# Kernel tuning notes

Hardware: AMD Instinct MI355X
Metric: run time of the kernel (lower is better)

The kernel has to match this reference:

```python
import jax, jax.numpy as jnp
import numpy as np

N = 100000   # nodes
E = 1200000  # edges
FIN = 128    # in_channels
H = 64       # hidden_channels
OUT = 1      # out_channels


def setup_inputs() -> dict:
    key = jax.random.key(0)
    ks = jax.random.split(key, 12)
    s = 0.05
    return {
        "x": jax.random.normal(ks[0], (N, FIN), jnp.float32),
        "edge_index": jax.random.randint(ks[1], (2, E), 0, N, dtype=jnp.int64),
        "W0": jax.random.normal(ks[2], (FIN, H), jnp.float32) * s,
        "b0": jnp.zeros((H,), jnp.float32),
        "W1": jax.random.normal(ks[3], (H, H), jnp.float32) * s,
        "b1": jnp.zeros((H,), jnp.float32),
        "W2": jax.random.normal(ks[4], (H, OUT), jnp.float32) * s,
        "b2": jnp.zeros((OUT,), jnp.float32),
        "Wm1": jax.random.normal(ks[5], (OUT, H), jnp.float32) * s,
        "bm1": jnp.zeros((H,), jnp.float32),
        "Wm2": jax.random.normal(ks[6], (H, OUT), jnp.float32) * s,
        "bm2": jnp.zeros((OUT,), jnp.float32),
    }


def reference(x, edge_index, W0, b0, W1, b1, W2, b2, Wm1, bm1, Wm2, bm2):
    # GCNConv (PyG default): add self-loops, symmetric normalization D^-1/2 A D^-1/2
    loop = jnp.arange(N, dtype=edge_index.dtype)
    src = jnp.concatenate([edge_index[0], loop])  # [E+N]
    dst = jnp.concatenate([edge_index[1], loop])
    deg = jax.ops.segment_sum(jnp.ones(E + N, jnp.float32), dst, num_segments=N)
    dinv = jax.lax.rsqrt(deg)  # deg >= 1 thanks to self-loops
    norm = dinv[src] * dinv[dst]  # [E+N]

    def conv(h, W, b):
        h = h @ W  # [N, d_out]
        msg = h[src] * norm[:, None]  # gather + scale, [E+N, d_out]
        return jax.ops.segment_sum(msg, dst, num_segments=N) + b

    h = jax.nn.relu(conv(x, W0, b0))   # input layer (dropout is identity in eval)
    h = jax.nn.relu(conv(h, W1, b1))   # hidden layer
    h = conv(h, W2, b2)                # output GCN layer -> [N, OUT]
    # MLP head
    h = jax.nn.relu(h @ Wm1 + bm1) @ Wm2 + bm2
    return h
```

## Files before the change

kernel.cpp:

```cpp
#include <hip/hip_runtime.h>
#include <hip/hip_fp16.h>
#include <math.h>

#define ELL_CAP 48
#define NBUCK 391
#define BCAP 3584

typedef _Float16 half8 __attribute__((ext_vector_type(8)));
typedef float floatx4 __attribute__((ext_vector_type(4)));


__device__ __forceinline__ __half2 u2h(unsigned u) {
  __half2 h; __builtin_memcpy(&h, &u, 4); return h;
}
__device__ __forceinline__ unsigned h2u(__half2 h) {
  unsigned u; __builtin_memcpy(&u, &h, 4); return u;
}


__global__ __launch_bounds__(1024) void k_bucket(const int* __restrict__ src,
                                                 const int* __restrict__ dst,
                                                 int* __restrict__ cursors,
                                                 int* __restrict__ buckets, int E) {
  __shared__ int hist[NBUCK];
  __shared__ int base[NBUCK];
  const int tid = threadIdx.x;
  for (int i = tid; i < NBUCK; i += 1024) hist[i] = 0;
  __syncthreads();

  const long s0 = (long)blockIdx.x * E / gridDim.x;
  const long s1 = (long)(blockIdx.x + 1) * E / gridDim.x;

  for (long e = s0 + tid; e < s1; e += 1024) atomicAdd(&hist[dst[e] >> 8], 1);
  __syncthreads();

  for (int i = tid; i < NBUCK; i += 1024) {
    int c = hist[i];
    base[i] = (c > 0) ? atomicAdd(&cursors[i], c) : 0;
    hist[i] = 0;
  }
  __syncthreads();

  for (long e = s0 + tid; e < s1; e += 1024) {
    int s = src[e], d = dst[e];
    int b = d >> 8;
    int pos = base[b] + atomicAdd(&hist[b], 1);
    if (pos < BCAP) buckets[(long)b * BCAP + pos] = ((d & 255) << 24) | s;
  }
}


__global__ __launch_bounds__(256) void k_ellbuild(const int* __restrict__ buckets,
                                                  const int* __restrict__ cursors,
                                                  int* __restrict__ cnt,
                                                  int* __restrict__ ell,
                                                  float* __restrict__ dinv,
                                                  int* __restrict__ remap,
                                                  __half* __restrict__ zrow, int n) {
  __shared__ int cnt_l[256];
  __shared__ int ell_l[256 * ELL_CAP];
  __shared__ int dh[64];
  __shared__ int dbase[64];
  const int b = blockIdx.x, tid = threadIdx.x;
  cnt_l[tid] = 0;
  if (tid < 64) dh[tid] = 0;
  if (b == 0 && tid < 64) zrow[tid] = __float2half(0.f);
  __syncthreads();

  int m = cursors[b];
  if (m > BCAP) m = BCAP;
  const int* bk = buckets + (long)b * BCAP;
  for (int i = tid; i < m; i += 256) {
    int p = bk[i];
    int ld = ((unsigned)p) >> 24;
    int pos = atomicAdd(&cnt_l[ld], 1);
    if (pos < ELL_CAP) ell_l[ld * ELL_CAP + pos] = p & 0xFFFFFF;
  }
  __syncthreads();

  const int d0 = b << 8;
  const int node = d0 + tid;
  const int rows = min(256, n - d0);
  int c = 0;
  if (tid < rows) {
    c = cnt_l[tid];
    if (c > ELL_CAP) c = ELL_CAP;
    cnt[node] = c;
    dinv[node] = 1.0f / sqrtf((float)(c + 1));
    atomicAdd(&dh[c], 1);
  }
  __syncthreads();
  if (tid == 0) {
    int s = 0;
    for (int i = 0; i < 64; ++i) { dbase[i] = s; s += dh[i]; }
  }
  __syncthreads();
  if (tid < rows) {
    int r = atomicAdd(&dbase[c], 1);
    remap[d0 + r] = node;
  }

  const int lim4 = rows * ELL_CAP / 4;
  int4* dst4 = (int4*)(ell + (long)d0 * ELL_CAP);
  const int4* src4 = (const int4*)ell_l;
  for (int i = tid; i < lim4; i += 256) dst4[i] = src4[i];
}


template <int K, bool RELU, bool IN_HALF>
__global__ __launch_bounds__(256) void k_gemm_mfma(const void* __restrict__ Xv,
                                                   const float* __restrict__ W,
                                                   const float* __restrict__ dinv,
                                                   __half* __restrict__ out, int n) {
  constexpr int SP = K + 8;
  constexpr int NS = K / 32;
  __shared__ __half Wl[64 * SP];
  const int tx = threadIdx.x;

  for (int idx = tx; idx < (K / 2) * 64; idx += 256) {
    int k2 = idx >> 6, col = idx & 63;
    __half2 h = __floats2half2_rn(W[(2 * k2) * 64 + col], W[(2 * k2 + 1) * 64 + col]);
    *(__half2*)&Wl[col * SP + 2 * k2] = h;
  }
  __syncthreads();

  const int lane = tx & 63;
  const int l15 = lane & 15;
  const int quad = lane >> 4;
  const long base = (long)blockIdx.x * 64 + (tx >> 6) * 16;

  long arow = base + l15;
  if (arow >= n) arow = n - 1;
  const float* Xf = (const float*)Xv;
  const __half* Xh = (const __half*)Xv;

  half8 afrag[NS];
#pragma unroll
  for (int s = 0; s < NS; ++s) {
    if constexpr (IN_HALF) {
      afrag[s] = *(const half8*)&Xh[arow * K + s * 32 + quad * 8];
    } else {
      float4 lo = *(const float4*)&Xf[arow * K + s * 32 + quad * 8];
      float4 hi = *(const float4*)&Xf[arow * K + s * 32 + quad * 8 + 4];
      half8 a;
      a[0] = (_Float16)lo.x; a[1] = (_Float16)lo.y;
      a[2] = (_Float16)lo.z; a[3] = (_Float16)lo.w;
      a[4] = (_Float16)hi.x; a[5] = (_Float16)hi.y;
      a[6] = (_Float16)hi.z; a[7] = (_Float16)hi.w;
      afrag[s] = a;
    }
    if (RELU) {
      unsigned short* u = (unsigned short*)&afrag[s];
#pragma unroll
      for (int j = 0; j < 8; ++j) u[j] = (u[j] & 0x8000) ? (unsigned short)0 : u[j];
    }
  }

  floatx4 acc[4];
#pragma unroll
  for (int t = 0; t < 4; ++t) acc[t] = (floatx4){0.f, 0.f, 0.f, 0.f};

#pragma unroll
  for (int s = 0; s < NS; ++s) {
#pragma unroll
    for (int t = 0; t < 4; ++t) {
      half8 bfrag = *(const half8*)&Wl[(t * 16 + l15) * SP + s * 32 + quad * 8];
      acc[t] = __builtin_amdgcn_mfma_f32_16x16x32_f16(afrag[s], bfrag, acc[t], 0, 0, 0);
    }
  }

#pragma unroll
  for (int r = 0; r < 4; ++r) {
    long node = base + quad * 4 + r;
    if (node < n) {
      float dv = dinv[node];
#pragma unroll
      for (int t = 0; t < 4; ++t)
        out[node * 64 + t * 16 + l15] = __float2half(acc[t][r] * dv);
    }
  }
}


template <typename EPI>
__device__ __forceinline__ void gather8(const __half* __restrict__ hs,
                                        const int* __restrict__ ell,
                                        const int* __restrict__ cnt,
                                        const float* __restrict__ dinv,
                                        const int* __restrict__ remap,
                                        int n, EPI epi) {
  const int tid = threadIdx.x;
  const int lane = tid & 63;
  const int l8 = lane & 7;
  const int wave = (blockIdx.x * 256 + tid) >> 6;
  const int slot = wave * 8 + (lane >> 3);
  const bool alive = slot < n;
  const int nd = alive ? remap[slot] : 0;
  const int c = alive ? cnt[nd] : 0;
  const float di = alive ? dinv[nd] : 0.f;
  const int* row = &ell[(long)nd * ELL_CAP];

  int s0 = (l8 < c) ? row[l8] : n;
  int s1 = (8 + l8 < c) ? row[8 + l8] : n;

  int cm = c;
  cm = max(cm, __shfl_xor(cm, 8, 64));
  cm = max(cm, __shfl_xor(cm, 16, 64));
  cm = max(cm, __shfl_xor(cm, 32, 64));
  const int nph = (cm + 7) >> 3;

  float accf[8];
  {
    float4 v = alive ? *(const float4*)&hs[(long)nd * 64 + l8 * 8]
                     : make_float4(0.f, 0.f, 0.f, 0.f);
    const unsigned* up = (const unsigned*)&v;
#pragma unroll
    for (int t = 0; t < 4; ++t) {
      float2 f = __half22float2(u2h(up[t]));
      accf[2 * t] = f.x; accf[2 * t + 1] = f.y;
    }
  }

  auto phase = [&](int reg) {
    int ss[8];
#pragma unroll
    for (int u = 0; u < 8; ++u) ss[u] = __shfl(reg, u, 8);
    float4 vv[8];
#pragma unroll
    for (int u = 0; u < 8; ++u) vv[u] = *(const float4*)&hs[(long)ss[u] * 64 + l8 * 8];
#pragma unroll
    for (int u = 0; u < 8; ++u) {
      const unsigned* up = (const unsigned*)&vv[u];
#pragma unroll
      for (int t = 0; t < 4; ++t) {
        float2 f = __half22float2(u2h(up[t]));
        accf[2 * t] += f.x; accf[2 * t + 1] += f.y;
      }
    }
  };

  if (nph > 0) phase(s0);
  if (nph > 1) phase(s1);
  for (int ph = 2; ph < nph; ++ph) {
    int reg = (ph * 8 + l8 < c) ? row[ph * 8 + l8] : n;
    phase(reg);
  }

  epi(accf, di, nd, l8, alive);
}

__global__ __launch_bounds__(256) void k_gather64x8(const __half* __restrict__ hs,
                                                    const int* __restrict__ ell,
                                                    const int* __restrict__ cnt,
                                                    const float* __restrict__ dinv,
                                                    const int* __restrict__ remap,
                                                    const float* __restrict__ b,
                                                    __half* __restrict__ agg, int n) {
  gather8(hs, ell, cnt, dinv, remap, n,
          [&](const float (&accf)[8], float di, int node, int l8, bool alive) {
    if (!alive) return;
    float4 bv0 = *(const float4*)&b[l8 * 8];
    float4 bv1 = *(const float4*)&b[l8 * 8 + 4];
    uint4 o;
    o.x = h2u(__floats2half2_rn(bv0.x + di * accf[0], bv0.y + di * accf[1]));
    o.y = h2u(__floats2half2_rn(bv0.z + di * accf[2], bv0.w + di * accf[3]));
    o.z = h2u(__floats2half2_rn(bv1.x + di * accf[4], bv1.y + di * accf[5]));
    o.w = h2u(__floats2half2_rn(bv1.z + di * accf[6], bv1.w + di * accf[7]));
    *(uint4*)&agg[(long)node * 64 + l8 * 8] = o;
  });
}

__global__ __launch_bounds__(256) void k_gather64x8_dot(const __half* __restrict__ hs,
                                                        const int* __restrict__ ell,
                                                        const int* __restrict__ cnt,
                                                        const float* __restrict__ dinv,
                                                        const int* __restrict__ remap,
                                                        const float* __restrict__ b1,
                                                        const float* __restrict__ W2,
                                                        float* __restrict__ h2s, int n) {
  if (blockIdx.x == 0 && threadIdx.x == 0) h2s[n] = 0.f;
  gather8(hs, ell, cnt, dinv, remap, n,
          [&](const float (&accf)[8], float di, int node, int l8, bool alive) {
    float4 bv0 = *(const float4*)&b1[l8 * 8];
    float4 bv1 = *(const float4*)&b1[l8 * 8 + 4];
    float4 wv0 = *(const float4*)&W2[l8 * 8];
    float4 wv1 = *(const float4*)&W2[l8 * 8 + 4];
    float part = fmaxf(bv0.x + di * accf[0], 0.f) * wv0.x;
    part = fmaf(fmaxf(bv0.y + di * accf[1], 0.f), wv0.y, part);
    part = fmaf(fmaxf(bv0.z + di * accf[2], 0.f), wv0.z, part);
    part = fmaf(fmaxf(bv0.w + di * accf[3], 0.f), wv0.w, part);
    part = fmaf(fmaxf(bv1.x + di * accf[4], 0.f), wv1.x, part);
    part = fmaf(fmaxf(bv1.y + di * accf[5], 0.f), wv1.y, part);
    part = fmaf(fmaxf(bv1.z + di * accf[6], 0.f), wv1.z, part);
    part = fmaf(fmaxf(bv1.w + di * accf[7], 0.f), wv1.w, part);
#pragma unroll
    for (int off = 1; off < 8; off <<= 1) part += __shfl_xor(part, off, 8);
    if (alive && l8 == 0) h2s[node] = di * part;
  });
}


__global__ __launch_bounds__(256) void k_gather1x8(const float* __restrict__ h2s,
                                                   const int* __restrict__ ell,
                                                   const int* __restrict__ cnt,
                                                   const float* __restrict__ dinv,
                                                   const int* __restrict__ remap,
                                                   const float* __restrict__ b2,
                                                   float* __restrict__ agg2, int n) {
  const int tid = threadIdx.x;
  const int lane = tid & 63;
  const int l8 = lane & 7;
  const int wave = (blockIdx.x * 256 + tid) >> 6;
  const int slot = wave * 8 + (lane >> 3);
  const bool alive = slot < n;
  const int nd = alive ? remap[slot] : 0;
  const int c = alive ? cnt[nd] : 0;
  const float di = alive ? dinv[nd] : 0.f;
  const int* row = &ell[(long)nd * ELL_CAP];

  int cm = c;
  cm = max(cm, __shfl_xor(cm, 8, 64));
  cm = max(cm, __shfl_xor(cm, 16, 64));
  cm = max(cm, __shfl_xor(cm, 32, 64));
  const int nph = (cm + 7) >> 3;

  float acc = (alive && l8 == 0) ? h2s[nd] : 0.f;
  for (int ph = 0; ph < nph; ++ph) {
    int j = ph * 8 + l8;
    int s = (j < c) ? row[j] : n;
    acc += h2s[s];
  }
#pragma unroll
  for (int off = 1; off < 8; off <<= 1) acc += __shfl_xor(acc, off, 8);
  if (alive && l8 == 0) agg2[nd] = b2[0] + di * acc;
}


__global__ void k_mlp(const float* __restrict__ agg2,
                      const float* __restrict__ Wm1, const float* __restrict__ bm1,
                      const float* __restrict__ Wm2, const float* __restrict__ bm2,
                      float* __restrict__ out, int n) {
  __shared__ float w1s[64], w2s[64], b1s[64];
  if (threadIdx.x < 64) {
    w1s[threadIdx.x] = Wm1[threadIdx.x];
    w2s[threadIdx.x] = Wm2[threadIdx.x];
    b1s[threadIdx.x] = bm1[threadIdx.x];
  }
  __syncthreads();
  int i = blockIdx.x * blockDim.x + threadIdx.x;
  if (i >= n) return;
  float s = agg2[i];
  float o = bm2[0];
#pragma unroll
  for (int j = 0; j < 64; ++j)
    o = fmaf(fmaxf(fmaf(s, w1s[j], b1s[j]), 0.f), w2s[j], o);
  out[i] = o;
}


extern "C" void kernel_launch(void* const* d_in, const int* in_sizes, int n_in,
                              void* d_out, int out_size, void* d_ws, size_t ws_size,
                              hipStream_t stream) {
  const float* x   = (const float*)d_in[0];
  const int*   ei  = (const int*)d_in[1];
  const float* W0  = (const float*)d_in[2];
  const float* b0  = (const float*)d_in[3];
  const float* W1  = (const float*)d_in[4];
  const float* b1  = (const float*)d_in[5];
  const float* W2  = (const float*)d_in[6];
  const float* b2  = (const float*)d_in[7];
  const float* Wm1 = (const float*)d_in[8];
  const float* bm1 = (const float*)d_in[9];
  const float* Wm2 = (const float*)d_in[10];
  const float* bm2 = (const float*)d_in[11];

  const int n = in_sizes[0] / 128;
  const int E = in_sizes[1] / 2;
  const int* src = ei;
  const int* dst = ei + E;

  float*  ws   = (float*)d_ws;
  float*  dinv = ws;
  int*    cnt  = (int*)(ws + n);
  int*    ell  = cnt + n;
  __half* bufA = (__half*)(ell + (size_t)n * ELL_CAP);
  __half* bufB = bufA + (size_t)(n + 1) * 64;
  float*  h2s  = (float*)(bufB + (size_t)n * 64);
  float*  agg2 = h2s + (n + 1);
  int*    remap = (int*)(agg2 + n);
  int*    cursors = (int*)(remap + n);
  int*    buckets = (int*)bufA;

  const int nb  = (n + 255) / 256;
  const int g8b = (((n + 7) / 8) + 3) / 4;
  const int mfb = (n + 63) / 64;

  hipMemsetAsync(cursors, 0, NBUCK * sizeof(int), stream);
  k_bucket<<<256, 1024, 0, stream>>>(src, dst, cursors, buckets, E);
  k_ellbuild<<<NBUCK, 256, 0, stream>>>(buckets, cursors, cnt, ell, dinv, remap,
                                        bufA + (size_t)n * 64, n);

  k_gemm_mfma<128, false, false><<<mfb, 256, 0, stream>>>(x, W0, dinv, bufA, n);
  k_gather64x8<<<g8b, 256, 0, stream>>>(bufA, ell, cnt, dinv, remap, b0, bufB, n);

  k_gemm_mfma<64, true, true><<<mfb, 256, 0, stream>>>(bufB, W1, dinv, bufA, n);
  k_gather64x8_dot<<<g8b, 256, 0, stream>>>(bufA, ell, cnt, dinv, remap, b1, W2, h2s, n);

  k_gather1x8<<<g8b, 256, 0, stream>>>(h2s, ell, cnt, dinv, remap, b2, agg2, n);
  k_mlp<<<nb, 256, 0, stream>>>(agg2, Wm1, bm1, Wm2, bm2, (float*)d_out, n);
}
```

Baseline: 234.2 us.

## Drop degree-sorted node remap, copy only used ELL slots, prefetch third index phase

Removes the per-block degree-sorting remap, so gather kernels handle nodes in natural order instead of grouping similar-degree nodes per wave. The ELL copy-out now writes only the int4 chunks each row actually uses rather than the full 48-wide row. The gather also preloads a third group of neighbour indices before the loop, and the bucket kernel launches half as many blocks. Together these cut preprocessing work and memory traffic, at the cost of more wave divergence in the gathers because wave-wide max degree now varies more.

```diff
diff --git a/kernel.cpp b/kernel.cpp
--- a/kernel.cpp
+++ b/kernel.cpp
@@ -55,15 +55,12 @@
                                                   int* __restrict__ cnt,
                                                   int* __restrict__ ell,
                                                   float* __restrict__ dinv,
-                                                  int* __restrict__ remap,
                                                   __half* __restrict__ zrow, int n) {
   __shared__ int cnt_l[256];
   __shared__ int ell_l[256 * ELL_CAP];
-  __shared__ int dh[64];
-  __shared__ int dbase[64];
+  __shared__ unsigned char lim4[256];
   const int b = blockIdx.x, tid = threadIdx.x;
   cnt_l[tid] = 0;
-  if (tid < 64) dh[tid] = 0;
   if (b == 0 && tid < 64) zrow[tid] = __float2half(0.f);
   __syncthreads();
 
@@ -81,29 +78,22 @@
   const int d0 = b << 8;
   const int node = d0 + tid;
   const int rows = min(256, n - d0);
-  int c = 0;
   if (tid < rows) {
-    c = cnt_l[tid];
+    int c = cnt_l[tid];
     if (c > ELL_CAP) c = ELL_CAP;
     cnt[node] = c;
     dinv[node] = 1.0f / sqrtf((float)(c + 1));
-    atomicAdd(&dh[c], 1);
-  }
-  __syncthreads();
-  if (tid == 0) {
-    int s = 0;
-    for (int i = 0; i < 64; ++i) { dbase[i] = s; s += dh[i]; }
-  }
-  __syncthreads();
-  if (tid < rows) {
-    int r = atomicAdd(&dbase[c], 1);
-    remap[d0 + r] = node;
-  }
-
-  const int lim4 = rows * ELL_CAP / 4;
+    lim4[tid] = (unsigned char)((c + 3) >> 2);
+  }
+  __syncthreads();
+
   int4* dst4 = (int4*)(ell + (long)d0 * ELL_CAP);
   const int4* src4 = (const int4*)ell_l;
-  for (int i = tid; i < lim4; i += 256) dst4[i] = src4[i];
+  const int tot = rows * 12;
+  for (int i = tid; i < tot; i += 256) {
+    int r = i / 12, w = i - r * 12;
+    if (w < (int)lim4[r]) dst4[i] = src4[i];
+  }
 }
 
 
@@ -187,21 +177,21 @@
                                         const int* __restrict__ ell,
                                         const int* __restrict__ cnt,
                                         const float* __restrict__ dinv,
-                                        const int* __restrict__ remap,
                                         int n, EPI epi) {
   const int tid = threadIdx.x;
   const int lane = tid & 63;
   const int l8 = lane & 7;
   const int wave = (blockIdx.x * 256 + tid) >> 6;
-  const int slot = wave * 8 + (lane >> 3);
-  const bool alive = slot < n;
-  const int nd = alive ? remap[slot] : 0;
+  const int node = wave * 8 + (lane >> 3);
+  const bool alive = node < n;
+  const int nd = alive ? node : 0;
   const int c = alive ? cnt[nd] : 0;
   const float di = alive ? dinv[nd] : 0.f;
   const int* row = &ell[(long)nd * ELL_CAP];
 
   int s0 = (l8 < c) ? row[l8] : n;
   int s1 = (8 + l8 < c) ? row[8 + l8] : n;
+  int s2 = (16 + l8 < c) ? row[16 + l8] : n;
 
   int cm = c;
   cm = max(cm, __shfl_xor(cm, 8, 64));
@@ -241,7 +231,8 @@
 
   if (nph > 0) phase(s0);
   if (nph > 1) phase(s1);
-  for (int ph = 2; ph < nph; ++ph) {
+  if (nph > 2) phase(s2);
+  for (int ph = 3; ph < nph; ++ph) {
     int reg = (ph * 8 + l8 < c) ? row[ph * 8 + l8] : n;
     phase(reg);
   }
@@ -253,10 +244,9 @@
                                                     const int* __restrict__ ell,
                                                     const int* __restrict__ cnt,
                                                     const float* __restrict__ dinv,
-                                                    const int* __restrict__ remap,
                                                     const float* __restrict__ b,
                                                     __half* __restrict__ agg, int n) {
-  gather8(hs, ell, cnt, dinv, remap, n,
+  gather8(hs, ell, cnt, dinv, n,
           [&](const float (&accf)[8], float di, int node, int l8, bool alive) {
     if (!alive) return;
     float4 bv0 = *(const float4*)&b[l8 * 8];
@@ -274,12 +264,11 @@
                                                         const int* __restrict__ ell,
                                                         const int* __restrict__ cnt,
                                                         const float* __restrict__ dinv,
-                                                        const int* __restrict__ remap,
                                                         const float* __restrict__ b1,
                                                         const float* __restrict__ W2,
                                                         float* __restrict__ h2s, int n) {
   if (blockIdx.x == 0 && threadIdx.x == 0) h2s[n] = 0.f;
-  gather8(hs, ell, cnt, dinv, remap, n,
+  gather8(hs, ell, cnt, dinv, n,
           [&](const float (&accf)[8], float di, int node, int l8, bool alive) {
     float4 bv0 = *(const float4*)&b1[l8 * 8];
     float4 bv1 = *(const float4*)&b1[l8 * 8 + 4];
@@ -304,16 +293,15 @@
                                                    const int* __restrict__ ell,
                                                    const int* __restrict__ cnt,
                                                    const float* __restrict__ dinv,
-                                                   const int* __restrict__ remap,
                                                    const float* __restrict__ b2,
                                                    float* __restrict__ agg2, int n) {
   const int tid = threadIdx.x;
   const int lane = tid & 63;
   const int l8 = lane & 7;
   const int wave = (blockIdx.x * 256 + tid) >> 6;
-  const int slot = wave * 8 + (lane >> 3);
-  const bool alive = slot < n;
-  const int nd = alive ? remap[slot] : 0;
+  const int node = wave * 8 + (lane >> 3);
+  const bool alive = node < n;
+  const int nd = alive ? node : 0;
   const int c = alive ? cnt[nd] : 0;
   const float di = alive ? dinv[nd] : 0.f;
   const int* row = &ell[(long)nd * ELL_CAP];
@@ -387,8 +375,7 @@
   __half* bufB = bufA + (size_t)(n + 1) * 64;
   float*  h2s  = (float*)(bufB + (size_t)n * 64);
   float*  agg2 = h2s + (n + 1);
-  int*    remap = (int*)(agg2 + n);
-  int*    cursors = (int*)(remap + n);
+  int*    cursors = (int*)(agg2 + n);
   int*    buckets = (int*)bufA;
 
   const int nb  = (n + 255) / 256;
@@ -396,16 +383,16 @@
   const int mfb = (n + 63) / 64;
 
   hipMemsetAsync(cursors, 0, NBUCK * sizeof(int), stream);
-  k_bucket<<<256, 1024, 0, stream>>>(src, dst, cursors, buckets, E);
-  k_ellbuild<<<NBUCK, 256, 0, stream>>>(buckets, cursors, cnt, ell, dinv, remap,
+  k_bucket<<<128, 1024, 0, stream>>>(src, dst, cursors, buckets, E);
+  k_ellbuild<<<NBUCK, 256, 0, stream>>>(buckets, cursors, cnt, ell, dinv,
                                         bufA + (size_t)n * 64, n);
 
   k_gemm_mfma<128, false, false><<<mfb, 256, 0, stream>>>(x, W0, dinv, bufA, n);
-  k_gather64x8<<<g8b, 256, 0, stream>>>(bufA, ell, cnt, dinv, remap, b0, bufB, n);
+  k_gather64x8<<<g8b, 256, 0, stream>>>(bufA, ell, cnt, dinv, b0, bufB, n);
 
   k_gemm_mfma<64, true, true><<<mfb, 256, 0, stream>>>(bufB, W1, dinv, bufA, n);
-  k_gather64x8_dot<<<g8b, 256, 0, stream>>>(bufA, ell, cnt, dinv, remap, b1, W2, h2s, n);
-
-  k_gather1x8<<<g8b, 256, 0, stream>>>(h2s, ell, cnt, dinv, remap, b2, agg2, n);
+  k_gather64x8_dot<<<g8b, 256, 0, stream>>>(bufA, ell, cnt, dinv, b1, W2, h2s, n);
+
+  k_gather1x8<<<g8b, 256, 0, stream>>>(h2s, ell, cnt, dinv, b2, agg2, n);
   k_mlp<<<nb, 256, 0, stream>>>(agg2, Wm1, bm1, Wm2, bm2, (float*)d_out, n);
 }
```

After: 220.3 us. -5.9%, faster.
